# Optimization experiments

Hardware: AMD Instinct MI355X
Metric: run time of the kernel (lower is better)

Reference implementation:

```python
import jax, jax.numpy as jnp
import numpy as np

DIM = 256
N_STATE = 8
DT_RANK = 16  # ceil(dim/16)
D_CONV = 4
HIDDEN = 128  # dim * rank_ratio
EPS = 1e-6


def rmsnorm(x, w):
    # matches torch: x / (||x||_2 / sqrt(d) + eps) * w
    norm = jnp.sqrt(jnp.sum(x * x, axis=-1, keepdims=True))
    return x / (norm / np.sqrt(x.shape[-1]) + EPS) * w


def dwconv1d(x, w, b, pad_l, pad_r):
    # x: (b, l, c); w: (c, 1, k) depthwise
    out = jax.lax.conv_general_dilated(
        x.transpose(0, 2, 1), w, window_strides=(1,),
        padding=[(pad_l, pad_r)], dimension_numbers=('NCH', 'OIH', 'NCH'),
        feature_group_count=w.shape[0])
    return (out + b[None, :, None]).transpose(0, 2, 1)


def selective_scan(x, delta, A, Bm, Cm, D):
    # x, delta: (b,l,d); A: (d,n); Bm, Cm: (b,l,n); D: (d,)
    dA = jnp.exp(delta[..., None] * A)                     # (b,l,d,n)
    dBx = (delta * x)[..., None] * Bm[:, :, None, :]       # (b,l,d,n)

    def step(h, inp):
        dA_t, dBx_t, C_t = inp
        h = dA_t * h + dBx_t                               # (b,d,n)
        y = jnp.einsum('bdn,bn->bd', h, C_t)
        return h, y

    h0 = jnp.zeros((x.shape[0],) + A.shape, dtype=x.dtype)
    _, ys = jax.lax.scan(step, h0,
                         (dA.transpose(1, 0, 2, 3), dBx.transpose(1, 0, 2, 3),
                          Cm.transpose(1, 0, 2)))
    return ys.transpose(1, 0, 2) + x * D                   # (b,l,d)


def mamba_branch(x, ctx, conv_w, conv_b, xproj_w, dtproj_w, dtproj_b, A_log, D):
    xc = jax.nn.silu(dwconv1d(x, conv_w, conv_b, D_CONV - 1, 0))  # causal conv
    x_dbl = ctx @ xproj_w.T                                  # (b,l,r+2n)
    dt, Bm, Cm = jnp.split(x_dbl, [DT_RANK, DT_RANK + N_STATE], axis=-1)
    delta = jax.nn.softplus(dt @ dtproj_w.T + dtproj_b)
    A = -jnp.exp(A_log)
    return selective_scan(xc, delta, A, Bm, Cm, D)


def setup_inputs() -> dict:
    key = jax.random.key(0)
    ks = jax.random.split(key, 24)
    B, L, D = 4, 64 * 64, DIM
    s = 0.02
    A_log_init = jnp.log(jnp.broadcast_to(jnp.arange(1, N_STATE + 1, dtype=jnp.float32), (D, N_STATE)))
    dt_bias = jnp.full((D,), jnp.log(jnp.expm1(0.01)), dtype=jnp.float32)
    inp = {
        'x0': jax.random.normal(ks[0], (B, L, D), jnp.float32),
        'x1': jax.random.normal(ks[1], (B, L, D), jnp.float32),
        'w_norm0': jnp.ones((D,), jnp.float32),
        'w_norm1': jnp.ones((D,), jnp.float32),
        'in_proj_w': jax.random.normal(ks[2], (2 * D, D), jnp.float32) * s,
        'conv_w_f': jax.random.normal(ks[3], (D, 1, D_CONV), jnp.float32) * 0.3,
        'conv_b_f': jnp.zeros((D,), jnp.float32),
        'xproj_w_f': jax.random.normal(ks[4], (DT_RANK + 2 * N_STATE, D), jnp.float32) * s,
        'dtproj_w_f': jax.random.normal(ks[5], (D, DT_RANK), jnp.float32) * 0.1,
        'dtproj_b_f': dt_bias,
        'A_log_f': A_log_init,
        'D_f': jnp.ones((D,), jnp.float32),
        'conv_w_bw': jax.random.normal(ks[6], (D, 1, D_CONV), jnp.float32) * 0.3,
        'conv_b_bw': jnp.zeros((D,), jnp.float32),
        'xproj_w_bw': jax.random.normal(ks[7], (DT_RANK + 2 * N_STATE, D), jnp.float32) * s,
        'dtproj_w_bw': jax.random.normal(ks[8], (D, DT_RANK), jnp.float32) * 0.1,
        'dtproj_b_bw': dt_bias,
        'A_log_bw': A_log_init,
        'D_bw': jnp.ones((D,), jnp.float32),
        'norm_y_w': jnp.ones((D,), jnp.float32),
        'out_proj_w': jax.random.normal(ks[9], (D, D), jnp.float32) * s,
        'fc1_w': jax.random.normal(ks[10], (HIDDEN, D), jnp.float32) * s,
        'dw_w': jax.random.normal(ks[11], (HIDDEN, 1, 3), jnp.float32) * 0.3,
        'dw_b': jnp.zeros((HIDDEN,), jnp.float32),
        'fc2_w': jax.random.normal(ks[12], (D, HIDDEN), jnp.float32) * s,
    }
    return inp


def reference(x0, x1, w_norm0, w_norm1, in_proj_w, conv_w_f, conv_b_f, xproj_w_f,
              dtproj_w_f, dtproj_b_f, A_log_f, D_f, conv_w_bw, conv_b_bw,
              xproj_w_bw, dtproj_w_bw, dtproj_b_bw, A_log_bw, D_bw, norm_y_w,
              out_proj_w, fc1_w, dw_w, dw_b, fc2_w):
    residual = x0
    h0 = rmsnorm(x0, w_norm0)
    h1 = rmsnorm(x1, w_norm1)
    # cross-Mamba: main stream x0 -> x,z; extra_emb x1 -> dt/B/C
    xz = h0 @ in_proj_w.T
    xin, z = jnp.split(xz, 2, axis=-1)
    y_f = mamba_branch(xin, h1, conv_w_f, conv_b_f, xproj_w_f, dtproj_w_f,
                       dtproj_b_f, A_log_f, D_f)
    y_b = jnp.flip(mamba_branch(jnp.flip(xin, 1), jnp.flip(h1, 1), conv_w_bw,
                                conv_b_bw, xproj_w_bw, dtproj_w_bw, dtproj_b_bw,
                                A_log_bw, D_bw), 1)
    y = (y_f + y_b) * 0.5          # if_devide_out=True (bidirectional)
    y = rmsnorm(y, norm_y_w)       # use_norm=True
    y = y * jax.nn.silu(z)
    x = y @ out_proj_w.T + residual
    # LowRankFeedForward (dropout = identity at eval)
    m = x @ fc1_w.T
    m = jax.nn.silu(dwconv1d(m, dw_w, dw_b, 1, 1))
    m = m @ fc2_w.T
    return x + m
```

## Files before the change

kernel.cpp:

```cpp
#include <hip/hip_runtime.h>
#include <math.h>
#include <cstddef>

#define BB 4
#define LL 4096
#define DD 256
#define NST 8
#define RANK 16
#define HID 128
#define BL (BB*LL)
#define BLD ((size_t)BL*DD)
#define CH 256
#define CLEN 16
#define XZS 512

typedef __bf16 bf16x8 __attribute__((ext_vector_type(8)));
typedef float  f32x4  __attribute__((ext_vector_type(4)));

__device__ __forceinline__ float siluf(float x){ return x / (1.f + __expf(-x)); }
__device__ __forceinline__ float softplus_fast(float x){
  float r = __logf(1.f + __expf(x));
  return x > 15.f ? x : r;
}
__device__ __forceinline__ unsigned short f2bf(float x){
  union { float f; unsigned u; } v; v.f = x;
  unsigned r = v.u + 0x7fffu + ((v.u >> 16) & 1u);
  return (unsigned short)(r >> 16);
}
__device__ __forceinline__ float bf2f(unsigned short u){
  union { unsigned u32; float f; } c; c.u32 = ((unsigned)u) << 16;
  return c.f;
}

#define GLD16(gp, lp) __builtin_amdgcn_global_load_lds( \
    (const __attribute__((address_space(1))) unsigned int*)(gp), \
    (__attribute__((address_space(3))) unsigned int*)(lp), 16, 0, 0)

#define LDSG(base, row, gq) \
  (*(const bf16x8*)((base) + ((((row) << 3) + ((gq) ^ ((row) & 7))) << 3)))

__global__ __launch_bounds__(256) void pre_kernel(
    const float* __restrict__ x0, const float* __restrict__ w0, unsigned short* __restrict__ o0b,
    const float* __restrict__ x1, const float* __restrict__ w1, unsigned short* __restrict__ o1b,
    const float* __restrict__ sA,
    const float* __restrict__ s0, const float* __restrict__ s1,
    const float* __restrict__ s2, const float* __restrict__ s3,
    const float* __restrict__ s4,
    unsigned short* __restrict__ d1, unsigned short* __restrict__ d2)
{
  int blk = blockIdx.x;
  if (blk < 8192){
    const float* x; const float* w; unsigned short* o; size_t tok;
    int wv = threadIdx.x >> 6, lane = threadIdx.x & 63;
    if (blk < 4096){ x = x0; w = w0; o = o0b; tok = (size_t)blk*4 + wv; }
    else           { x = x1; w = w1; o = o1b; tok = (size_t)(blk-4096)*4 + wv; }
    float4 v = ((const float4*)(x + tok*DD))[lane];
    float s = v.x*v.x + v.y*v.y + v.z*v.z + v.w*v.w;
    #pragma unroll
    for (int m = 1; m < 64; m <<= 1) s += __shfl_xor(s, m, 64);
    float scale = 1.f / (sqrtf(s) * (1.f/16.f) + 1e-6f);
    float4 wvv = ((const float4*)w)[lane];
    ushort4 r;
    r.x = f2bf(v.x*scale*wvv.x); r.y = f2bf(v.y*scale*wvv.y);
    r.z = f2bf(v.z*scale*wvv.z); r.w = f2bf(v.w*scale*wvv.w);
    ((ushort4*)(o + tok*DD))[lane] = r;
    return;
  }
  int i = (blk - 8192)*256 + threadIdx.x;
  if (i >= 278528) return;
  if (i < 131072){ d1[i] = f2bf(sA[i]); return; }
  int j = i - 131072;
  float v;
  if (j < 8192)        v = s0[j];
  else if (j < 16384)  v = s1[j - 8192];
  else if (j < 81920)  v = s2[j - 16384];
  else if (j < 114688) v = s3[j - 81920];
  else                 v = s4[j - 114688];
  d2[j] = f2bf(v);
}

template<int EPI>
__global__ __launch_bounds__(256) void gemm_mfma(
    const unsigned short* __restrict__ A, const unsigned short* __restrict__ Bw,
    float* __restrict__ C, const float* __restrict__ Add,
    unsigned short* __restrict__ Cb, int M, int ldc, int K)
{
  constexpr int BK = 64;
  __shared__ __align__(16) unsigned short AsL[64*64];
  __shared__ __align__(16) unsigned short BsL[64*64];
  int tid  = threadIdx.x;
  int row0 = blockIdx.x * 64;
  int col0 = blockIdx.y * 64;
  int wave = tid >> 6, lane = tid & 63;
  int wm = (wave >> 1) * 32, wn = (wave & 1) * 32;
  int lm = lane & 15, kq = lane >> 4;

  int q0 = wave*128 + lane, q1 = q0 + 64;
  int ra = q0 >> 3, ga = (q0 & 7) ^ (ra & 7);
  int rb = q1 >> 3, gb = (q1 & 7) ^ (rb & 7);
  const unsigned short* A0 = A  + (size_t)(row0 + ra)*K + ga*8;
  const unsigned short* A1 = A  + (size_t)(row0 + rb)*K + gb*8;
  const unsigned short* B0 = Bw + (size_t)(col0 + ra)*K + ga*8;
  const unsigned short* B1 = Bw + (size_t)(col0 + rb)*K + gb*8;
  unsigned short* lA0 = AsL + wave*1024;
  unsigned short* lB0 = BsL + wave*1024;

  f32x4 acc[2][2];
  #pragma unroll
  for (int i = 0; i < 2; i++)
    #pragma unroll
    for (int j = 0; j < 2; j++) acc[i][j] = (f32x4){0.f,0.f,0.f,0.f};

  for (int k0 = 0; k0 < K; k0 += BK){
    GLD16(A0 + k0, lA0);       GLD16(A1 + k0, lA0 + 512);
    GLD16(B0 + k0, lB0);       GLD16(B1 + k0, lB0 + 512);
    __syncthreads();
    #pragma unroll
    for (int ks = 0; ks < 2; ks++){
      bf16x8 af[2], bfv[2];
      #pragma unroll
      for (int i = 0; i < 2; i++) af[i]  = LDSG(AsL, wm + i*16 + lm, ks*4 + kq);
      #pragma unroll
      for (int j = 0; j < 2; j++) bfv[j] = LDSG(BsL, wn + j*16 + lm, ks*4 + kq);
      #pragma unroll
      for (int i = 0; i < 2; i++)
        #pragma unroll
        for (int j = 0; j < 2; j++)
          acc[i][j] = __builtin_amdgcn_mfma_f32_16x16x32_bf16(af[i], bfv[j], acc[i][j], 0, 0, 0);
    }
    __syncthreads();
  }

  #pragma unroll
  for (int i = 0; i < 2; i++){
    int rbase = row0 + wm + i*16 + kq*4;
    #pragma unroll
    for (int j = 0; j < 2; j++){
      int col = col0 + wn + j*16 + lm;
      #pragma unroll
      for (int r = 0; r < 4; r++){
        size_t idx = (size_t)(rbase + r)*ldc + col;
        float v = acc[i][j][r];
        if constexpr (EPI == 2) v += Add[idx];
        if constexpr (EPI != 3) C[idx] = v;
        if constexpr (EPI == 3) Cb[idx] = f2bf(v);
      }
    }
  }
}

__global__ __launch_bounds__(256) void gemm_xzxp(
    const unsigned short* __restrict__ A0i, const unsigned short* __restrict__ A1i,
    const unsigned short* __restrict__ B0i, const unsigned short* __restrict__ B1i,
    unsigned short* __restrict__ Cxz, float* __restrict__ Cxd)
{
  constexpr int BK = 64, K = 256;
  __shared__ __align__(16) unsigned short AsL[64*64];
  __shared__ __align__(16) unsigned short BsL[64*64];
  int tid  = threadIdx.x;
  bool xp  = (blockIdx.y == 8);
  const unsigned short* A  = xp ? A1i : A0i;
  const unsigned short* Bw = xp ? B1i : B0i;
  int row0 = blockIdx.x * 64;
  int col0 = xp ? 0 : blockIdx.y * 64;
  int wave = tid >> 6, lane = tid & 63;
  int wm = (wave >> 1) * 32, wn = (wave & 1) * 32;
  int lm = lane & 15, kq = lane >> 4;

  int q0 = wave*128 + lane, q1 = q0 + 64;
  int ra = q0 >> 3, ga = (q0 & 7) ^ (ra & 7);
  int rb = q1 >> 3, gb = (q1 & 7) ^ (rb & 7);
  const unsigned short* A0 = A  + (size_t)(row0 + ra)*K + ga*8;
  const unsigned short* A1 = A  + (size_t)(row0 + rb)*K + gb*8;
  const unsigned short* B0 = Bw + (size_t)(col0 + ra)*K + ga*8;
  const unsigned short* B1 = Bw + (size_t)(col0 + rb)*K + gb*8;
  unsigned short* lA0 = AsL + wave*1024;
  unsigned short* lB0 = BsL + wave*1024;

  f32x4 acc[2][2];
  #pragma unroll
  for (int i = 0; i < 2; i++)
    #pragma unroll
    for (int j = 0; j < 2; j++) acc[i][j] = (f32x4){0.f,0.f,0.f,0.f};

  for (int k0 = 0; k0 < K; k0 += BK){
    GLD16(A0 + k0, lA0);       GLD16(A1 + k0, lA0 + 512);
    GLD16(B0 + k0, lB0);       GLD16(B1 + k0, lB0 + 512);
    __syncthreads();
    #pragma unroll
    for (int ks = 0; ks < 2; ks++){
      bf16x8 af[2], bfv[2];
      #pragma unroll
      for (int i = 0; i < 2; i++) af[i]  = LDSG(AsL, wm + i*16 + lm, ks*4 + kq);
      #pragma unroll
      for (int j = 0; j < 2; j++) bfv[j] = LDSG(BsL, wn + j*16 + lm, ks*4 + kq);
      #pragma unroll
      for (int i = 0; i < 2; i++)
        #pragma unroll
        for (int j = 0; j < 2; j++)
          acc[i][j] = __builtin_amdgcn_mfma_f32_16x16x32_bf16(af[i], bfv[j], acc[i][j], 0, 0, 0);
    }
    __syncthreads();
  }

  #pragma unroll
  for (int i = 0; i < 2; i++){
    int rbase = row0 + wm + i*16 + kq*4;
    #pragma unroll
    for (int j = 0; j < 2; j++){
      int col = col0 + wn + j*16 + lm;
      #pragma unroll
      for (int r = 0; r < 4; r++){
        float v = acc[i][j][r];
        if (xp) Cxd[(size_t)(rbase + r)*64  + col] = v;
        else    Cxz[(size_t)(rbase + r)*XZS + col] = f2bf(v);
      }
    }
  }
}

__global__ __launch_bounds__(256) void gemm_fc1(
    const float* __restrict__ A, const unsigned short* __restrict__ Bw,
    float* __restrict__ C)
{
  constexpr int BK = 64, PAD = 8, K = 256, LDC = 128;
  __shared__ __align__(16) unsigned short As[64][BK+PAD];
  __shared__ __align__(16) unsigned short BsL[64*64];
  int tid  = threadIdx.x;
  int row0 = blockIdx.x * 64;
  int col0 = blockIdx.y * 64;
  int wave = tid >> 6, lane = tid & 63;
  int wm = (wave >> 1) * 32, wn = (wave & 1) * 32;
  int lm = lane & 15, kq = lane >> 4;
  int sr = tid >> 2, sc16 = (tid & 3) * 16;

  int q0 = wave*128 + lane, q1 = q0 + 64;
  int ra = q0 >> 3, ga = (q0 & 7) ^ (ra & 7);
  int rb = q1 >> 3, gb = (q1 & 7) ^ (rb & 7);
  const unsigned short* B0 = Bw + (size_t)(col0 + ra)*K + ga*8;
  const unsigned short* B1 = Bw + (size_t)(col0 + rb)*K + gb*8;
  unsigned short* lB0 = BsL + wave*1024;

  f32x4 acc[2][2];
  #pragma unroll
  for (int i = 0; i < 2; i++)
    #pragma unroll
    for (int j = 0; j < 2; j++) acc[i][j] = (f32x4){0.f,0.f,0.f,0.f};

  for (int k0 = 0; k0 < K; k0 += BK){
    GLD16(B0 + k0, lB0);       GLD16(B1 + k0, lB0 + 512);
    const float* ap = &A[(size_t)(row0 + sr)*K + k0 + sc16];
    #pragma unroll
    for (int q = 0; q < 4; q++){
      float4 f = *(const float4*)(ap + q*4);
      ushort4 u; u.x = f2bf(f.x); u.y = f2bf(f.y); u.z = f2bf(f.z); u.w = f2bf(f.w);
      *(ushort4*)&As[sr][sc16 + q*4] = u;
    }
    __syncthreads();
    #pragma unroll
    for (int ks = 0; ks < 2; ks++){
      bf16x8 af[2], bfv[2];
      #pragma unroll
      for (int i = 0; i < 2; i++) af[i]  = *(const bf16x8*)&As[wm + i*16 + lm][ks*32 + kq*8];
      #pragma unroll
      for (int j = 0; j < 2; j++) bfv[j] = LDSG(BsL, wn + j*16 + lm, ks*4 + kq);
      #pragma unroll
      for (int i = 0; i < 2; i++)
        #pragma unroll
        for (int j = 0; j < 2; j++)
          acc[i][j] = __builtin_amdgcn_mfma_f32_16x16x32_bf16(af[i], bfv[j], acc[i][j], 0, 0, 0);
    }
    __syncthreads();
  }

  #pragma unroll
  for (int i = 0; i < 2; i++){
    int rbase = row0 + wm + i*16 + kq*4;
    #pragma unroll
    for (int j = 0; j < 2; j++){
      int col = col0 + wn + j*16 + lm;
      #pragma unroll
      for (int r = 0; r < 4; r++)
        C[(size_t)(rbase + r)*LDC + col] = acc[i][j][r];
    }
  }
}

__global__ __launch_bounds__(256) void gemm_fc2dw(
    const float* __restrict__ m1, const unsigned short* __restrict__ Bw,
    const float* __restrict__ dww, const float* __restrict__ dwb,
    float* __restrict__ C)
{
  constexpr int BK = 64, PAD = 8, K = 128, LDC = 256;
  __shared__ __align__(16) unsigned short As[64][BK+PAD];
  __shared__ __align__(16) unsigned short BsL[64*64];
  __shared__ float wS[HID*3];
  __shared__ float bS[HID];
  int tid  = threadIdx.x;
  if (tid < HID){
    bS[tid] = dwb[tid];
    wS[tid*3+0] = dww[tid*3+0];
    wS[tid*3+1] = dww[tid*3+1];
    wS[tid*3+2] = dww[tid*3+2];
  }
  __syncthreads();

  int row0 = blockIdx.x * 64;
  int col0 = blockIdx.y * 64;
  int wave = tid >> 6, lane = tid & 63;
  int wm = (wave >> 1) * 32, wn = (wave & 1) * 32;
  int lm = lane & 15, kq = lane >> 4;
  int r16 = tid >> 4, cc = (tid & 15) * 4;

  int q0 = wave*128 + lane, q1 = q0 + 64;
  int ra = q0 >> 3, ga = (q0 & 7) ^ (ra & 7);
  int rb = q1 >> 3, gb = (q1 & 7) ^ (rb & 7);
  const unsigned short* B0 = Bw + (size_t)(col0 + ra)*K + ga*8;
  const unsigned short* B1 = Bw + (size_t)(col0 + rb)*K + gb*8;
  unsigned short* lB0 = BsL + wave*1024;

  f32x4 acc[2][2];
  #pragma unroll
  for (int i = 0; i < 2; i++)
    #pragma unroll
    for (int j = 0; j < 2; j++) acc[i][j] = (f32x4){0.f,0.f,0.f,0.f};

  for (int k0 = 0; k0 < K; k0 += BK){
    GLD16(B0 + k0, lB0);       GLD16(B1 + k0, lB0 + 512);
    #pragma unroll
    for (int pp = 0; pp < 4; pp++){
      int r = pp*16 + r16;
      int t = row0 + r;
      int tl = t & (LL-1);
      int c = k0 + cc;
      const float* mrow = &m1[(size_t)t*HID + c];
      float4 vm = *(const float4*)mrow;
      float4 vp = (tl > 0)      ? *(const float4*)(mrow - HID) : (float4){0,0,0,0};
      float4 vn = (tl < LL-1)   ? *(const float4*)(mrow + HID) : (float4){0,0,0,0};
      float a0 = bS[c+0] + wS[(c+0)*3]*vp.x + wS[(c+0)*3+1]*vm.x + wS[(c+0)*3+2]*vn.x;
      float a1 = bS[c+1] + wS[(c+1)*3]*vp.y + wS[(c+1)*3+1]*vm.y + wS[(c+1)*3+2]*vn.y;
      float a2 = bS[c+2] + wS[(c+2)*3]*vp.z + wS[(c+2)*3+1]*vm.z + wS[(c+2)*3+2]*vn.z;
      float a3 = bS[c+3] + wS[(c+3)*3]*vp.w + wS[(c+3)*3+1]*vm.w + wS[(c+3)*3+2]*vn.w;
      ushort4 u;
      u.x = f2bf(siluf(a0)); u.y = f2bf(siluf(a1));
      u.z = f2bf(siluf(a2)); u.w = f2bf(siluf(a3));
      *(ushort4*)&As[r][cc] = u;
    }
    __syncthreads();
    #pragma unroll
    for (int ks = 0; ks < 2; ks++){
      bf16x8 af[2], bfv[2];
      #pragma unroll
      for (int i = 0; i < 2; i++) af[i]  = *(const bf16x8*)&As[wm + i*16 + lm][ks*32 + kq*8];
      #pragma unroll
      for (int j = 0; j < 2; j++) bfv[j] = LDSG(BsL, wn + j*16 + lm, ks*4 + kq);
      #pragma unroll
      for (int i = 0; i < 2; i++)
        #pragma unroll
        for (int j = 0; j < 2; j++)
          acc[i][j] = __builtin_amdgcn_mfma_f32_16x16x32_bf16(af[i], bfv[j], acc[i][j], 0, 0, 0);
    }
    __syncthreads();
  }

  #pragma unroll
  for (int i = 0; i < 2; i++){
    int rbase = row0 + wm + i*16 + kq*4;
    #pragma unroll
    for (int j = 0; j < 2; j++){
      int col = col0 + wn + j*16 + lm;
      #pragma unroll
      for (int r = 0; r < 4; r++){
        size_t idx = (size_t)(rbase + r)*LDC + col;
        C[idx] = C[idx] + acc[i][j][r];
      }
    }
  }
}

__global__ __launch_bounds__(256) void front_kernel(
    const unsigned short* __restrict__ xz,
    const float* __restrict__ xd,
    const float* __restrict__ cwf, const float* __restrict__ cbf,
    const float* __restrict__ cwb, const float* __restrict__ cbb,
    const float* __restrict__ dtwf, const float* __restrict__ dtbf,
    const float* __restrict__ dtwb, const float* __restrict__ dtbb,
    const float* __restrict__ Alogf, const float* __restrict__ Alogb,
    const float* __restrict__ Dfp, const float* __restrict__ Dbp,
    unsigned int* __restrict__ xde,
    float* __restrict__ Sp, float* __restrict__ Hout)
{
  int chunk = blockIdx.x, b = blockIdx.y, dir = blockIdx.z;
  int s0 = chunk*CLEN;
  int d  = threadIdx.x;

  __shared__ float sdt[CLEN][16];
  __shared__ float sB [CLEN][8];
  __shared__ float sC [CLEN][8];
  #pragma unroll
  for (int e = threadIdx.x; e < CLEN*32; e += 256){
    int lt = e >> 5, col = e & 31;
    int pos = s0 + lt;
    int row = dir ? (LL-1-pos) : pos;
    float v = xd[((size_t)b*LL + row)*64 + dir*32 + col];
    if (col < 16)      sdt[lt][col]    = v;
    else if (col < 24) sB [lt][col-16] = v;
    else               sC [lt][col-24] = v;
  }
  __syncthreads();

  float4 cw = ((const float4*)(dir ? cwb : cwf))[d];
  float cb  = (dir ? cbb : cbf)[d];
  const float* dtw = (dir ? dtwb : dtwf) + d*RANK;
  float4 w0 = ((const float4*)dtw)[0], w1 = ((const float4*)dtw)[1];
  float4 w2 = ((const float4*)dtw)[2], w3 = ((const float4*)dtw)[3];
  float dtb = (dir ? dtbb : dtbf)[d];
  float Dd  = (dir ? Dbp : Dfp)[d];

  const unsigned short* xp = xz + (size_t)b*LL*XZS + d;
  #define LDX(pos) ((pos) >= 0 ? bf2f(xp[(size_t)(dir ? (LL-1-(pos)) : (pos))*XZS]) : 0.f)

  float xv[CLEN+3];
  xv[0] = LDX(s0-3); xv[1] = LDX(s0-2); xv[2] = LDX(s0-1);
  #pragma unroll
  for (int i = 0; i < CLEN; i++) xv[3+i] = LDX(s0+i);
  #undef LDX

  unsigned packX[CLEN];
  #pragma unroll
  for (int i = 0; i < CLEN; i++){
    float xc = cb;
    xc = fmaf(cw.x, xv[i],   xc); xc = fmaf(cw.y, xv[i+1], xc);
    xc = fmaf(cw.z, xv[i+2], xc); xc = fmaf(cw.w, xv[i+3], xc);
    xc = siluf(xc);
    const float* dt = &sdt[i][0];
    float de = dtb;
    de = fmaf(dt[0],w0.x, fmaf(dt[1],w0.y, fmaf(dt[2],w0.z, fmaf(dt[3],w0.w, de))));
    de = fmaf(dt[4],w1.x, fmaf(dt[5],w1.y, fmaf(dt[6],w1.z, fmaf(dt[7],w1.w, de))));
    de = fmaf(dt[8],w2.x, fmaf(dt[9],w2.y, fmaf(dt[10],w2.z, fmaf(dt[11],w2.w, de))));
    de = fmaf(dt[12],w3.x, fmaf(dt[13],w3.y, fmaf(dt[14],w3.z, fmaf(dt[15],w3.w, de))));
    de = softplus_fast(de);
    packX[i] = (unsigned)f2bf(xc) | ((unsigned)f2bf(de) << 16);
  }

  const float* Alog = dir ? Alogb : Alogf;
  float A[NST];
  bool fast = true;
  #pragma unroll
  for (int n = 0; n < NST; n++){
    A[n] = -__expf(Alog[d*NST + n]);
    fast = fast && (fabsf(A[n] + (float)(n+1)) < 1e-3f);
  }
  float h[NST];
  #pragma unroll
  for (int n = 0; n < NST; n++) h[n] = 0.f;
  float S = 0.f;

  unsigned int* xout = xde + ((size_t)(dir*BB + b)*LL + s0)*DD + d;

  if (fast){
    #pragma unroll
    for (int t = 0; t < CLEN; t++){
      unsigned pk = packX[t];
      float xc = bf2f((unsigned short)(pk & 0xffffu));
      float de = bf2f((unsigned short)(pk >> 16));
      S += de;
      float dux = de * xc;
      const float* Bv = &sB[t][0];
      const float* Cv = &sC[t][0];
      float e1 = __expf(-de);
      float dA = e1;
      float acc = xc * Dd;
      h[0] = fmaf(dA, h[0], dux*Bv[0]); acc = fmaf(h[0], Cv[0], acc); dA *= e1;
      h[1] = fmaf(dA, h[1], dux*Bv[1]); acc = fmaf(h[1], Cv[1], acc); dA *= e1;
      h[2] = fmaf(dA, h[2], dux*Bv[2]); acc = fmaf(h[2], Cv[2], acc); dA *= e1;
      h[3] = fmaf(dA, h[3], dux*Bv[3]); acc = fmaf(h[3], Cv[3], acc); dA *= e1;
      h[4] = fmaf(dA, h[4], dux*Bv[4]); acc = fmaf(h[4], Cv[4], acc); dA *= e1;
      h[5] = fmaf(dA, h[5], dux*Bv[5]); acc = fmaf(h[5], Cv[5], acc); dA *= e1;
      h[6] = fmaf(dA, h[6], dux*Bv[6]); acc = fmaf(h[6], Cv[6], acc); dA *= e1;
      h[7] = fmaf(dA, h[7], dux*Bv[7]); acc = fmaf(h[7], Cv[7], acc);
      xout[(size_t)t*DD] = (pk & 0xffff0000u) | (unsigned)f2bf(acc);
    }
  } else {
    #pragma unroll
    for (int t = 0; t < CLEN; t++){
      unsigned pk = packX[t];
      float xc = bf2f((unsigned short)(pk & 0xffffu));
      float de = bf2f((unsigned short)(pk >> 16));
      S += de;
      float dux = de * xc;
      const float* Bv = &sB[t][0];
      const float* Cv = &sC[t][0];
      float acc = xc * Dd;
      #pragma unroll
      for (int n = 0; n < NST; n++){
        h[n] = fmaf(__expf(de*A[n]), h[n], dux*Bv[n]);
        acc = fmaf(h[n], Cv[n], acc);
      }
      xout[(size_t)t*DD] = (pk & 0xffff0000u) | (unsigned)f2bf(acc);
    }
  }

  size_t ob = ((((size_t)dir*CH + chunk)*BB + b)*DD + d)*NST;
  float4 h0v, h1v;
  h0v.x=h[0]; h0v.y=h[1]; h0v.z=h[2]; h0v.w=h[3];
  h1v.x=h[4]; h1v.y=h[5]; h1v.z=h[6]; h1v.w=h[7];
  *(float4*)&Hout[ob]   = h0v; *(float4*)&Hout[ob+4] = h1v;
  Sp[((size_t)(dir*CH + chunk)*BB + b)*DD + d] = S;
}

__global__ __launch_bounds__(64) void scan_p2(
    const float* __restrict__ Sp, float* H,
    const float* __restrict__ Alogf, const float* __restrict__ Alogb)
{
  const int SEGC = CH/8;
  int blk = blockIdx.x;
  int d   = blk & (DD-1);
  int b   = (blk >> 8) & (BB-1);
  int dir = blk >> 10;
  int t   = threadIdx.x;
  int seg = t >> 3, n = t & 7;
  float A = -__expf((dir ? Alogb : Alogf)[d*NST + n]);

  const size_t sstr = (size_t)BB*DD;
  const size_t hstr = (size_t)BB*DD*NST;
  size_t sb = (size_t)dir*CH*sstr + (size_t)b*DD + d;
  size_t hb = (size_t)dir*CH*hstr + ((size_t)b*DD + d)*NST + n;
  int c0 = seg*SEGC;

  float pv[SEGC], hv[SEGC];
  #pragma unroll
  for (int k = 0; k < SEGC; k++){
    pv[k] = Sp[sb + (size_t)(c0+k)*sstr];
    hv[k] = H [hb + (size_t)(c0+k)*hstr];
  }
  float h = 0.f, Ss = 0.f;
  #pragma unroll
  for (int k = 0; k < SEGC; k++){
    Ss += pv[k];
    pv[k] = __expf(pv[k]*A);
    h = fmaf(pv[k], h, hv[k]);
  }
  float pi = __expf(Ss*A), hi = h;
  #pragma unroll
  for (int off = 8; off < 64; off <<= 1){
    float hprev = __shfl_up(hi, off, 64);
    float pprev = __shfl_up(pi, off, 64);
    if (t >= off){ hi = fmaf(pi, hprev, hi); pi *= pprev; }
  }
  float hin = __shfl_up(hi, 8, 64);
  h = (seg == 0) ? 0.f : hin;
  #pragma unroll
  for (int k = 0; k < SEGC; k++){
    size_t idx = hb + (size_t)(c0+k)*hstr;
    H[idx] = h;
    h = fmaf(pv[k], h, hv[k]);
  }
}

__global__ __launch_bounds__(256) void back_kernel(
    const unsigned int* __restrict__ xde,
    const float* __restrict__ xd,
    const float* __restrict__ Alogf, const float* __restrict__ Alogb,
    const float* __restrict__ Hin,
    const unsigned short* __restrict__ xz,
    const float* __restrict__ wn,
    unsigned short* __restrict__ outb)
{
  int c  = blockIdx.x, b = blockIdx.y;
  int cbk = CH-1-c;
  int d  = threadIdx.x;
  int T0 = c*CLEN;
  int Pb = cbk*CLEN;

  __shared__ float sCf[CLEN][8], sCb[CLEN][8];
  __shared__ float red[CLEN][4];
  __shared__ float sscale[CLEN];
  {
    int k  = threadIdx.x & 7;
    int lt = (threadIdx.x >> 3) & 15;
    if (threadIdx.x < 128)
      sCf[lt][k] = xd[((size_t)b*LL + T0 + lt)*64 + 24 + k];
    else
      sCb[lt][k] = xd[((size_t)b*LL + (T0 + 15 - lt))*64 + 56 + k];
  }
  __syncthreads();

  float Af[NST], Ab[NST];
  bool fast = true;
  #pragma unroll
  for (int n = 0; n < NST; n++){
    Af[n] = -__expf(Alogf[d*NST + n]);
    Ab[n] = -__expf(Alogb[d*NST + n]);
    fast = fast && (fabsf(Af[n] + (float)(n+1)) < 1e-3f)
                && (fabsf(Ab[n] + (float)(n+1)) < 1e-3f);
  }

  float vf[CLEN];

  {
    float hn[NST];
    size_t ib = (((size_t)c*BB + b)*DD + d)*NST;
    float4 a0 = *(const float4*)&Hin[ib];
    float4 a1 = *(const float4*)&Hin[ib+4];
    hn[0]=a0.x; hn[1]=a0.y; hn[2]=a0.z; hn[3]=a0.w;
    hn[4]=a1.x; hn[5]=a1.y; hn[6]=a1.z; hn[7]=a1.w;
    const unsigned int* p = xde + ((size_t)b*LL + T0)*DD + d;
    unsigned int pk[CLEN];
    #pragma unroll
    for (int t = 0; t < CLEN; t++) pk[t] = p[(size_t)t*DD];
    float S = 0.f;
    if (fast){
      #pragma unroll
      for (int t = 0; t < CLEN; t++){
        float y0 = bf2f((unsigned short)(pk[t] & 0xffffu));
        float de = bf2f((unsigned short)(pk[t] >> 16));
        S += de;
        float E = __expf(-S);
        float q = E;
        float corr = q * (hn[0]*sCf[t][0]);
        q *= E; corr = fmaf(q, hn[1]*sCf[t][1], corr);
        q *= E; corr = fmaf(q, hn[2]*sCf[t][2], corr);
        q *= E; corr = fmaf(q, hn[3]*sCf[t][3], corr);
        q *= E; corr = fmaf(q, hn[4]*sCf[t][4], corr);
        q *= E; corr = fmaf(q, hn[5]*sCf[t][5], corr);
        q *= E; corr = fmaf(q, hn[6]*sCf[t][6], corr);
        q *= E; corr = fmaf(q, hn[7]*sCf[t][7], corr);
        vf[t] = y0 + corr;
      }
    } else {
      #pragma unroll
      for (int t = 0; t < CLEN; t++){
        float y0 = bf2f((unsigned short)(pk[t] & 0xffffu));
        float de = bf2f((unsigned short)(pk[t] >> 16));
        S += de;
        float corr = 0.f;
        #pragma unroll
        for (int n = 0; n < NST; n++)
          corr = fmaf(__expf(S*Af[n]), hn[n]*sCf[t][n], corr);
        vf[t] = y0 + corr;
      }
    }
  }

  {
    float hn[NST];
    size_t ib = ((((size_t)CH + cbk)*BB + b)*DD + d)*NST;
    float4 a0 = *(const float4*)&Hin[ib];
    float4 a1 = *(const float4*)&Hin[ib+4];
    hn[0]=a0.x; hn[1]=a0.y; hn[2]=a0.z; hn[3]=a0.w;
    hn[4]=a1.x; hn[5]=a1.y; hn[6]=a1.z; hn[7]=a1.w;
    const unsigned int* p = xde + ((size_t)(BB + b)*LL + Pb)*DD + d;
    unsigned int pk[CLEN];
    #pragma unroll
    for (int t = 0; t < CLEN; t++) pk[t] = p[(size_t)t*DD];
    float S = 0.f;
    if (fast){
      #pragma unroll
      for (int t = 0; t < CLEN; t++){
        float y0 = bf2f((unsigned short)(pk[t] & 0xffffu));
        float de = bf2f((unsigned short)(pk[t] >> 16));
        S += de;
        float E = __expf(-S);
        float q = E;
        float corr = q * (hn[0]*sCb[t][0]);
        q *= E; corr = fmaf(q, hn[1]*sCb[t][1], corr);
        q *= E; corr = fmaf(q, hn[2]*sCb[t][2], corr);
        q *= E; corr = fmaf(q, hn[3]*sCb[t][3], corr);
        q *= E; corr = fmaf(q, hn[4]*sCb[t][4], corr);
        q *= E; corr = fmaf(q, hn[5]*sCb[t][5], corr);
        q *= E; corr = fmaf(q, hn[6]*sCb[t][6], corr);
        q *= E; corr = fmaf(q, hn[7]*sCb[t][7], corr);
        int j = 15 - t;
        vf[j] = 0.5f*(vf[j] + y0 + corr);
      }
    } else {
      #pragma unroll
      for (int t = 0; t < CLEN; t++){
        float y0 = bf2f((unsigned short)(pk[t] & 0xffffu));
        float de = bf2f((unsigned short)(pk[t] >> 16));
        S += de;
        float corr = 0.f;
        #pragma unroll
        for (int n = 0; n < NST; n++)
          corr = fmaf(__expf(S*Ab[n]), hn[n]*sCb[t][n], corr);
        int j = 15 - t;
        vf[j] = 0.5f*(vf[j] + y0 + corr);
      }
    }
  }

  int wave = d >> 6, lane = d & 63;
  #pragma unroll
  for (int j = 0; j < CLEN; j++){
    float s = vf[j]*vf[j];
    #pragma unroll
    for (int m = 1; m < 64; m <<= 1) s += __shfl_xor(s, m, 64);
    if (lane == 0) red[j][wave] = s;
  }
  __syncthreads();
  if (d < CLEN){
    float s = red[d][0] + red[d][1] + red[d][2] + red[d][3];
    sscale[d] = 1.f / (sqrtf(s)*(1.f/16.f) + 1e-6f);
  }
  __syncthreads();

  float wd = wn[d];
  #pragma unroll
  for (int j = 0; j < CLEN; j++){
    size_t tok = (size_t)b*LL + T0 + j;
    float z = bf2f(xz[tok*XZS + 256 + d]);
    outb[tok*DD + d] = f2bf(vf[j]*sscale[j]*wd*siluf(z));
  }
}

extern "C" void kernel_launch(void* const* d_in, const int* in_sizes, int n_in,
                              void* d_out, int out_size, void* d_ws, size_t ws_size,
                              hipStream_t stream)
{
  const float* x0        = (const float*)d_in[0];
  const float* x1        = (const float*)d_in[1];
  const float* w_norm0   = (const float*)d_in[2];
  const float* w_norm1   = (const float*)d_in[3];
  const float* in_proj_w = (const float*)d_in[4];
  const float* conv_w_f  = (const float*)d_in[5];
  const float* conv_b_f  = (const float*)d_in[6];
  const float* xproj_w_f = (const float*)d_in[7];
  const float* dtproj_w_f= (const float*)d_in[8];
  const float* dtproj_b_f= (const float*)d_in[9];
  const float* A_log_f   = (const float*)d_in[10];
  const float* D_f       = (const float*)d_in[11];
  const float* conv_w_bw = (const float*)d_in[12];
  const float* conv_b_bw = (const float*)d_in[13];
  const float* xproj_w_bw= (const float*)d_in[14];
  const float* dtproj_w_bw=(const float*)d_in[15];
  const float* dtproj_b_bw=(const float*)d_in[16];
  const float* A_log_bw  = (const float*)d_in[17];
  const float* D_bw      = (const float*)d_in[18];
  const float* norm_y_w  = (const float*)d_in[19];
  const float* out_proj_w= (const float*)d_in[20];
  const float* fc1_w     = (const float*)d_in[21];
  const float* dw_w      = (const float*)d_in[22];
  const float* dw_b      = (const float*)d_in[23];
  const float* fc2_w     = (const float*)d_in[24];
  float* out = (float*)d_out;
  float* ws  = (float*)d_ws;

  float* r0 = ws + 0*BLD;
  float* r1 = ws + 1*BLD;
  float* r2 = ws + 2*BLD;
  float* r3 = ws + 3*BLD;
  float* r4 = ws + 4*BLD;
  float* r5 = ws + 5*BLD;
  float* r6 = ws + 6*BLD;
  float* r7 = ws + 7*BLD;

  unsigned short* h0b   = (unsigned short*)r0;
  unsigned short* h1b   = (unsigned short*)r1;
  unsigned short* xz_b  = (unsigned short*)r2;
  float*          xd    = r3;
  unsigned int*   xde   = (unsigned int*)r4;
  unsigned short* wbuf1 = (unsigned short*)r6;
  float* Hout = r6;
  float* Hin  = Hout;
  const size_t SPLANE = (size_t)2*CH*BB*DD;
  float* Sp   = r7 + (BLD - SPLANE);
  unsigned short* ycomb_b = (unsigned short*)r0;
  unsigned short* wbuf2   = (unsigned short*)r7;
  unsigned short* wb_xp   = wbuf2;
  unsigned short* wb_out  = wbuf2 + 16384;
  unsigned short* wb_fc1  = wbuf2 + 81920;
  unsigned short* wb_fc2  = wbuf2 + 114688;
  float*          m1      = r4;

  pre_kernel<<<dim3(9280), 256, 0, stream>>>(
      x0, w_norm0, h0b, x1, w_norm1, h1b,
      in_proj_w, xproj_w_f, xproj_w_bw, out_proj_w, fc1_w, fc2_w, wbuf1, wbuf2);

  gemm_xzxp<<<dim3(BL/64, 9), 256, 0, stream>>>(
      h0b, h1b, wbuf1, wb_xp, xz_b, xd);

  front_kernel<<<dim3(CH, BB, 2), 256, 0, stream>>>(
      xz_b, xd, conv_w_f, conv_b_f, conv_w_bw, conv_b_bw,
      dtproj_w_f, dtproj_b_f, dtproj_w_bw, dtproj_b_bw,
      A_log_f, A_log_bw, D_f, D_bw, xde, Sp, Hout);

  scan_p2<<<dim3(2*BB*DD), 64, 0, stream>>>(Sp, Hout, A_log_f, A_log_bw);

  back_kernel<<<dim3(CH, BB), 256, 0, stream>>>(
      xde, xd, A_log_f, A_log_bw, Hin, xz_b, norm_y_w, ycomb_b);

  gemm_mfma<2><<<dim3(BL/64, 4), 256, 0, stream>>>(
      ycomb_b, wb_out, out, x0, nullptr, BL, 256, 256);

  gemm_fc1<<<dim3(BL/64, 2), 256, 0, stream>>>(out, wb_fc1, m1);

  gemm_fc2dw<<<dim3(BL/64, 4), 256, 0, stream>>>(m1, wb_fc2, dw_w, dw_b, out);
}
```

Baseline: 248.6 us.

## Fuse chunked scan phases into one persistent kernel with grid barriers

Merges the front (per-chunk local scan), the inter-chunk prefix pass and the back (correction + norm) kernels into a single 1024-block kernel that synchronises with software grid barriers. Per-chunk packed y/delta values stay in registers across the barriers instead of round-tripping through a global xde buffer, and two kernel launches are removed. It relies on all 1024 blocks being co-resident (launch_bounds 256,4), which risks deadlock if occupancy is lower, and it leaves most blocks idle during the middle phase and adds register pressure.

Result: slower. 670.1 us (+169.5%).

```diff
diff --git a/kernel.cpp b/kernel.cpp
--- a/kernel.cpp
+++ b/kernel.cpp
@@ -39,6 +39,24 @@
 #define LDSG(base, row, gq) \
   (*(const bf16x8*)((base) + ((((row) << 3) + ((gq) ^ ((row) & 7))) << 3)))
 
+__device__ __forceinline__ void grid_barrier(unsigned* cnt, unsigned* gen, unsigned nb){
+  __syncthreads();
+  if (threadIdx.x == 0){
+    __threadfence();
+    unsigned g = __hip_atomic_load(gen, __ATOMIC_RELAXED, __HIP_MEMORY_SCOPE_AGENT);
+    unsigned a = __hip_atomic_fetch_add(cnt, 1u, __ATOMIC_ACQ_REL, __HIP_MEMORY_SCOPE_AGENT);
+    if (a == nb - 1u){
+      __hip_atomic_store(cnt, 0u, __ATOMIC_RELAXED, __HIP_MEMORY_SCOPE_AGENT);
+      __hip_atomic_fetch_add(gen, 1u, __ATOMIC_RELEASE, __HIP_MEMORY_SCOPE_AGENT);
+    } else {
+      while (__hip_atomic_load(gen, __ATOMIC_ACQUIRE, __HIP_MEMORY_SCOPE_AGENT) == g)
+        __builtin_amdgcn_s_sleep(8);
+    }
+    __threadfence();
+  }
+  __syncthreads();
+}
+
 __global__ __launch_bounds__(256) void pre_kernel(
     const float* __restrict__ x0, const float* __restrict__ w0, unsigned short* __restrict__ o0b,
     const float* __restrict__ x1, const float* __restrict__ w1, unsigned short* __restrict__ o1b,
@@ -46,9 +64,11 @@
     const float* __restrict__ s0, const float* __restrict__ s1,
     const float* __restrict__ s2, const float* __restrict__ s3,
     const float* __restrict__ s4,
-    unsigned short* __restrict__ d1, unsigned short* __restrict__ d2)
+    unsigned short* __restrict__ d1, unsigned short* __restrict__ d2,
+    unsigned* __restrict__ bar)
 {
   int blk = blockIdx.x;
+  if (blk == 8192 && threadIdx.x < 2) bar[threadIdx.x] = 0;
   if (blk < 8192){
     const float* x; const float* w; unsigned short* o; size_t tok;
     int wv = threadIdx.x >> 6, lane = threadIdx.x & 63;
@@ -378,7 +398,7 @@
   }
 }
 
-__global__ __launch_bounds__(256) void front_kernel(
+__global__ __launch_bounds__(256, 4) void fused_scan(
     const unsigned short* __restrict__ xz,
     const float* __restrict__ xd,
     const float* __restrict__ cwf, const float* __restrict__ cbf,
@@ -387,205 +407,188 @@
     const float* __restrict__ dtwb, const float* __restrict__ dtbb,
     const float* __restrict__ Alogf, const float* __restrict__ Alogb,
     const float* __restrict__ Dfp, const float* __restrict__ Dbp,
-    unsigned int* __restrict__ xde,
-    float* __restrict__ Sp, float* __restrict__ Hout)
+    const float* __restrict__ wn,
+    unsigned short* __restrict__ outb,
+    float* __restrict__ Sp, float* H, unsigned* bar)
 {
-  int chunk = blockIdx.x, b = blockIdx.y, dir = blockIdx.z;
-  int s0 = chunk*CLEN;
-  int d  = threadIdx.x;
+  int blk = blockIdx.x;
+  int c   = blk >> 2;
+  int b   = blk & 3;
+  int d   = threadIdx.x;
+  int cbk = CH-1-c;
 
   __shared__ float sdt[CLEN][16];
   __shared__ float sB [CLEN][8];
-  __shared__ float sC [CLEN][8];
-  #pragma unroll
-  for (int e = threadIdx.x; e < CLEN*32; e += 256){
-    int lt = e >> 5, col = e & 31;
-    int pos = s0 + lt;
-    int row = dir ? (LL-1-pos) : pos;
-    float v = xd[((size_t)b*LL + row)*64 + dir*32 + col];
-    if (col < 16)      sdt[lt][col]    = v;
-    else if (col < 24) sB [lt][col-16] = v;
-    else               sC [lt][col-24] = v;
-  }
-  __syncthreads();
-
-  float4 cw = ((const float4*)(dir ? cwb : cwf))[d];
-  float cb  = (dir ? cbb : cbf)[d];
-  const float* dtw = (dir ? dtwb : dtwf) + d*RANK;
-  float4 w0 = ((const float4*)dtw)[0], w1 = ((const float4*)dtw)[1];
-  float4 w2 = ((const float4*)dtw)[2], w3 = ((const float4*)dtw)[3];
-  float dtb = (dir ? dtbb : dtbf)[d];
-  float Dd  = (dir ? Dbp : Dfp)[d];
-
-  const unsigned short* xp = xz + (size_t)b*LL*XZS + d;
-  #define LDX(pos) ((pos) >= 0 ? bf2f(xp[(size_t)(dir ? (LL-1-(pos)) : (pos))*XZS]) : 0.f)
-
-  float xv[CLEN+3];
-  xv[0] = LDX(s0-3); xv[1] = LDX(s0-2); xv[2] = LDX(s0-1);
-  #pragma unroll
-  for (int i = 0; i < CLEN; i++) xv[3+i] = LDX(s0+i);
-  #undef LDX
-
-  unsigned packX[CLEN];
-  #pragma unroll
-  for (int i = 0; i < CLEN; i++){
-    float xc = cb;
-    xc = fmaf(cw.x, xv[i],   xc); xc = fmaf(cw.y, xv[i+1], xc);
-    xc = fmaf(cw.z, xv[i+2], xc); xc = fmaf(cw.w, xv[i+3], xc);
-    xc = siluf(xc);
-    const float* dt = &sdt[i][0];
-    float de = dtb;
-    de = fmaf(dt[0],w0.x, fmaf(dt[1],w0.y, fmaf(dt[2],w0.z, fmaf(dt[3],w0.w, de))));
-    de = fmaf(dt[4],w1.x, fmaf(dt[5],w1.y, fmaf(dt[6],w1.z, fmaf(dt[7],w1.w, de))));
-    de = fmaf(dt[8],w2.x, fmaf(dt[9],w2.y, fmaf(dt[10],w2.z, fmaf(dt[11],w2.w, de))));
-    de = fmaf(dt[12],w3.x, fmaf(dt[13],w3.y, fmaf(dt[14],w3.z, fmaf(dt[15],w3.w, de))));
-    de = softplus_fast(de);
-    packX[i] = (unsigned)f2bf(xc) | ((unsigned)f2bf(de) << 16);
-  }
-
-  const float* Alog = dir ? Alogb : Alogf;
-  float A[NST];
-  bool fast = true;
-  #pragma unroll
-  for (int n = 0; n < NST; n++){
-    A[n] = -__expf(Alog[d*NST + n]);
-    fast = fast && (fabsf(A[n] + (float)(n+1)) < 1e-3f);
-  }
-  float h[NST];
-  #pragma unroll
-  for (int n = 0; n < NST; n++) h[n] = 0.f;
-  float S = 0.f;
-
-  unsigned int* xout = xde + ((size_t)(dir*BB + b)*LL + s0)*DD + d;
-
-  if (fast){
-    #pragma unroll
-    for (int t = 0; t < CLEN; t++){
-      unsigned pk = packX[t];
-      float xc = bf2f((unsigned short)(pk & 0xffffu));
-      float de = bf2f((unsigned short)(pk >> 16));
-      S += de;
-      float dux = de * xc;
-      const float* Bv = &sB[t][0];
-      const float* Cv = &sC[t][0];
-      float e1 = __expf(-de);
-      float dA = e1;
-      float acc = xc * Dd;
-      h[0] = fmaf(dA, h[0], dux*Bv[0]); acc = fmaf(h[0], Cv[0], acc); dA *= e1;
-      h[1] = fmaf(dA, h[1], dux*Bv[1]); acc = fmaf(h[1], Cv[1], acc); dA *= e1;
-      h[2] = fmaf(dA, h[2], dux*Bv[2]); acc = fmaf(h[2], Cv[2], acc); dA *= e1;
-      h[3] = fmaf(dA, h[3], dux*Bv[3]); acc = fmaf(h[3], Cv[3], acc); dA *= e1;
-      h[4] = fmaf(dA, h[4], dux*Bv[4]); acc = fmaf(h[4], Cv[4], acc); dA *= e1;
-      h[5] = fmaf(dA, h[5], dux*Bv[5]); acc = fmaf(h[5], Cv[5], acc); dA *= e1;
-      h[6] = fmaf(dA, h[6], dux*Bv[6]); acc = fmaf(h[6], Cv[6], acc); dA *= e1;
-      h[7] = fmaf(dA, h[7], dux*Bv[7]); acc = fmaf(h[7], Cv[7], acc);
-      xout[(size_t)t*DD] = (pk & 0xffff0000u) | (unsigned)f2bf(acc);
-    }
-  } else {
-    #pragma unroll
-    for (int t = 0; t < CLEN; t++){
-      unsigned pk = packX[t];
-      float xc = bf2f((unsigned short)(pk & 0xffffu));
-      float de = bf2f((unsigned short)(pk >> 16));
-      S += de;
-      float dux = de * xc;
-      const float* Bv = &sB[t][0];
-      const float* Cv = &sC[t][0];
-      float acc = xc * Dd;
-      #pragma unroll
-      for (int n = 0; n < NST; n++){
-        h[n] = fmaf(__expf(de*A[n]), h[n], dux*Bv[n]);
-        acc = fmaf(h[n], Cv[n], acc);
-      }
-      xout[(size_t)t*DD] = (pk & 0xffff0000u) | (unsigned)f2bf(acc);
-    }
-  }
-
-  size_t ob = ((((size_t)dir*CH + chunk)*BB + b)*DD + d)*NST;
-  float4 h0v, h1v;
-  h0v.x=h[0]; h0v.y=h[1]; h0v.z=h[2]; h0v.w=h[3];
-  h1v.x=h[4]; h1v.y=h[5]; h1v.z=h[6]; h1v.w=h[7];
-  *(float4*)&Hout[ob]   = h0v; *(float4*)&Hout[ob+4] = h1v;
-  Sp[((size_t)(dir*CH + chunk)*BB + b)*DD + d] = S;
-}
-
-__global__ __launch_bounds__(64) void scan_p2(
-    const float* __restrict__ Sp, float* H,
-    const float* __restrict__ Alogf, const float* __restrict__ Alogb)
-{
-  const int SEGC = CH/8;
-  int blk = blockIdx.x;
-  int d   = blk & (DD-1);
-  int b   = (blk >> 8) & (BB-1);
-  int dir = blk >> 10;
-  int t   = threadIdx.x;
-  int seg = t >> 3, n = t & 7;
-  float A = -__expf((dir ? Alogb : Alogf)[d*NST + n]);
-
-  const size_t sstr = (size_t)BB*DD;
-  const size_t hstr = (size_t)BB*DD*NST;
-  size_t sb = (size_t)dir*CH*sstr + (size_t)b*DD + d;
-  size_t hb = (size_t)dir*CH*hstr + ((size_t)b*DD + d)*NST + n;
-  int c0 = seg*SEGC;
-
-  float pv[SEGC], hv[SEGC];
-  #pragma unroll
-  for (int k = 0; k < SEGC; k++){
-    pv[k] = Sp[sb + (size_t)(c0+k)*sstr];
-    hv[k] = H [hb + (size_t)(c0+k)*hstr];
-  }
-  float h = 0.f, Ss = 0.f;
-  #pragma unroll
-  for (int k = 0; k < SEGC; k++){
-    Ss += pv[k];
-    pv[k] = __expf(pv[k]*A);
-    h = fmaf(pv[k], h, hv[k]);
-  }
-  float pi = __expf(Ss*A), hi = h;
-  #pragma unroll
-  for (int off = 8; off < 64; off <<= 1){
-    float hprev = __shfl_up(hi, off, 64);
-    float pprev = __shfl_up(pi, off, 64);
-    if (t >= off){ hi = fmaf(pi, hprev, hi); pi *= pprev; }
-  }
-  float hin = __shfl_up(hi, 8, 64);
-  h = (seg == 0) ? 0.f : hin;
-  #pragma unroll
-  for (int k = 0; k < SEGC; k++){
-    size_t idx = hb + (size_t)(c0+k)*hstr;
-    H[idx] = h;
-    h = fmaf(pv[k], h, hv[k]);
-  }
-}
-
-__global__ __launch_bounds__(256) void back_kernel(
-    const unsigned int* __restrict__ xde,
-    const float* __restrict__ xd,
-    const float* __restrict__ Alogf, const float* __restrict__ Alogb,
-    const float* __restrict__ Hin,
-    const unsigned short* __restrict__ xz,
-    const float* __restrict__ wn,
-    unsigned short* __restrict__ outb)
-{
-  int c  = blockIdx.x, b = blockIdx.y;
-  int cbk = CH-1-c;
-  int d  = threadIdx.x;
-  int T0 = c*CLEN;
-  int Pb = cbk*CLEN;
-
-  __shared__ float sCf[CLEN][8], sCb[CLEN][8];
+  __shared__ float sCf[CLEN][8];
+  __shared__ float sCb[CLEN][8];
   __shared__ float red[CLEN][4];
   __shared__ float sscale[CLEN];
+
+  unsigned pkF[CLEN], pkB[CLEN];
+
+  auto run_front = [&](int chunk, int dirv, float (&sCx)[CLEN][8], unsigned* pk){
+    int s0 = chunk*CLEN;
+    __syncthreads();
+    #pragma unroll
+    for (int e = d; e < CLEN*32; e += 256){
+      int lt = e >> 5, col = e & 31;
+      int pos = s0 + lt;
+      int row = dirv ? (LL-1-pos) : pos;
+      float v = xd[((size_t)b*LL + row)*64 + dirv*32 + col];
+      if (col < 16)      sdt[lt][col]    = v;
+      else if (col < 24) sB [lt][col-16] = v;
+      else               sCx[lt][col-24] = v;
+    }
+    __syncthreads();
+
+    float4 cw = ((const float4*)(dirv ? cwb : cwf))[d];
+    float cb  = (dirv ? cbb : cbf)[d];
+    const float* dtw = (dirv ? dtwb : dtwf) + d*RANK;
+    float4 w0 = ((const float4*)dtw)[0], w1 = ((const float4*)dtw)[1];
+    float4 w2 = ((const float4*)dtw)[2], w3 = ((const float4*)dtw)[3];
+    float dtb = (dirv ? dtbb : dtbf)[d];
+    float Dd  = (dirv ? Dbp : Dfp)[d];
+
+    const unsigned short* xp = xz + (size_t)b*LL*XZS + d;
+    #define LDX(pos) ((pos) >= 0 ? bf2f(xp[(size_t)(dirv ? (LL-1-(pos)) : (pos))*XZS]) : 0.f)
+    float xv[CLEN+3];
+    xv[0] = LDX(s0-3); xv[1] = LDX(s0-2); xv[2] = LDX(s0-1);
+    #pragma unroll
+    for (int i = 0; i < CLEN; i++) xv[3+i] = LDX(s0+i);
+    #undef LDX
+
+    #pragma unroll
+    for (int i = 0; i < CLEN; i++){
+      float xc = cb;
+      xc = fmaf(cw.x, xv[i],   xc); xc = fmaf(cw.y, xv[i+1], xc);
+      xc = fmaf(cw.z, xv[i+2], xc); xc = fmaf(cw.w, xv[i+3], xc);
+      xc = siluf(xc);
+      const float* dt = &sdt[i][0];
+      float de = dtb;
+      de = fmaf(dt[0],w0.x, fmaf(dt[1],w0.y, fmaf(dt[2],w0.z, fmaf(dt[3],w0.w, de))));
+      de = fmaf(dt[4],w1.x, fmaf(dt[5],w1.y, fmaf(dt[6],w1.z, fmaf(dt[7],w1.w, de))));
+      de = fmaf(dt[8],w2.x, fmaf(dt[9],w2.y, fmaf(dt[10],w2.z, fmaf(dt[11],w2.w, de))));
+      de = fmaf(dt[12],w3.x, fmaf(dt[13],w3.y, fmaf(dt[14],w3.z, fmaf(dt[15],w3.w, de))));
+      de = softplus_fast(de);
+      pk[i] = (unsigned)f2bf(xc) | ((unsigned)f2bf(de) << 16);
+    }
+
+    const float* Alog = dirv ? Alogb : Alogf;
+    float A[NST];
+    bool fast = true;
+    #pragma unroll
+    for (int n = 0; n < NST; n++){
+      A[n] = -__expf(Alog[d*NST + n]);
+      fast = fast && (fabsf(A[n] + (float)(n+1)) < 1e-3f);
+    }
+    float h[NST];
+    #pragma unroll
+    for (int n = 0; n < NST; n++) h[n] = 0.f;
+    float S = 0.f;
+
+    if (fast){
+      #pragma unroll
+      for (int t = 0; t < CLEN; t++){
+        unsigned pkv = pk[t];
+        float xc = bf2f((unsigned short)(pkv & 0xffffu));
+        float de = bf2f((unsigned short)(pkv >> 16));
+        S += de;
+        float dux = de * xc;
+        const float* Bv = &sB[t][0];
+        const float* Cv = &sCx[t][0];
+        float e1 = __expf(-de);
+        float dA = e1;
+        float acc = xc * Dd;
+        h[0] = fmaf(dA, h[0], dux*Bv[0]); acc = fmaf(h[0], Cv[0], acc); dA *= e1;
+        h[1] = fmaf(dA, h[1], dux*Bv[1]); acc = fmaf(h[1], Cv[1], acc); dA *= e1;
+        h[2] = fmaf(dA, h[2], dux*Bv[2]); acc = fmaf(h[2], Cv[2], acc); dA *= e1;
+        h[3] = fmaf(dA, h[3], dux*Bv[3]); acc = fmaf(h[3], Cv[3], acc); dA *= e1;
+        h[4] = fmaf(dA, h[4], dux*Bv[4]); acc = fmaf(h[4], Cv[4], acc); dA *= e1;
+        h[5] = fmaf(dA, h[5], dux*Bv[5]); acc = fmaf(h[5], Cv[5], acc); dA *= e1;
+        h[6] = fmaf(dA, h[6], dux*Bv[6]); acc = fmaf(h[6], Cv[6], acc); dA *= e1;
+        h[7] = fmaf(dA, h[7], dux*Bv[7]); acc = fmaf(h[7], Cv[7], acc);
+        pk[t] = (pkv & 0xffff0000u) | (unsigned)f2bf(acc);
+      }
+    } else {
+      #pragma unroll
+      for (int t = 0; t < CLEN; t++){
+        unsigned pkv = pk[t];
+        float xc = bf2f((unsigned short)(pkv & 0xffffu));
+        float de = bf2f((unsigned short)(pkv >> 16));
+        S += de;
+        float dux = de * xc;
+        const float* Bv = &sB[t][0];
+        const float* Cv = &sCx[t][0];
+        float acc = xc * Dd;
+        #pragma unroll
+        for (int n = 0; n < NST; n++){
+          h[n] = fmaf(__expf(de*A[n]), h[n], dux*Bv[n]);
+          acc = fmaf(h[n], Cv[n], acc);
+        }
+        pk[t] = (pkv & 0xffff0000u) | (unsigned)f2bf(acc);
+      }
+    }
+
+    size_t ob = ((((size_t)dirv*CH + chunk)*BB + b)*DD + d)*NST;
+    float4 h0v, h1v;
+    h0v.x=h[0]; h0v.y=h[1]; h0v.z=h[2]; h0v.w=h[3];
+    h1v.x=h[4]; h1v.y=h[5]; h1v.z=h[6]; h1v.w=h[7];
+    *(float4*)&H[ob]   = h0v; *(float4*)&H[ob+4] = h1v;
+    Sp[((size_t)(dirv*CH + chunk)*BB + b)*DD + d] = S;
+  };
+
+  run_front(c,   0, sCf, pkF);
+  run_front(cbk, 1, sCb, pkB);
+
+  grid_barrier(bar, bar+1, CH*BB);
+
   {
-    int k  = threadIdx.x & 7;
-    int lt = (threadIdx.x >> 3) & 15;
-    if (threadIdx.x < 128)
-      sCf[lt][k] = xd[((size_t)b*LL + T0 + lt)*64 + 24 + k];
-    else
-      sCb[lt][k] = xd[((size_t)b*LL + (T0 + 15 - lt))*64 + 56 + k];
-  }
-  __syncthreads();
-
+    int wave = d >> 6, lane = d & 63;
+    if (wave < 2){
+      const int SEGC = CH/8;
+      int u   = blk*2 + wave;
+      int d2  = u & (DD-1);
+      int b2  = (u >> 8) & (BB-1);
+      int dir2= u >> 10;
+      int seg = lane >> 3, n = lane & 7;
+      float A = -__expf((dir2 ? Alogb : Alogf)[d2*NST + n]);
+      const size_t sstr = (size_t)BB*DD;
+      const size_t hstr = (size_t)BB*DD*NST;
+      size_t sb = (size_t)dir2*CH*sstr + (size_t)b2*DD + d2;
+      size_t hb = (size_t)dir2*CH*hstr + ((size_t)b2*DD + d2)*NST + n;
+      int c0 = seg*SEGC;
+
+      float hv[SEGC];
+      float h = 0.f, Ss = 0.f;
+      #pragma unroll
+      for (int k = 0; k < SEGC; k++){
+        float s = Sp[sb + (size_t)(c0+k)*sstr];
+        hv[k]  = H [hb + (size_t)(c0+k)*hstr];
+        Ss += s;
+        h = fmaf(__expf(s*A), h, hv[k]);
+      }
+      float pi = __expf(Ss*A), hi = h;
+      #pragma unroll
+      for (int off = 8; off < 64; off <<= 1){
+        float hprev = __shfl_up(hi, off, 64);
+        float pprev = __shfl_up(pi, off, 64);
+        if (lane >= off){ hi = fmaf(pi, hprev, hi); pi *= pprev; }
+      }
+      float hin = __shfl_up(hi, 8, 64);
+      h = (seg == 0) ? 0.f : hin;
+      #pragma unroll
+      for (int k = 0; k < SEGC; k++){
+        float s = Sp[sb + (size_t)(c0+k)*sstr];
+        size_t hix = hb + (size_t)(c0+k)*hstr;
+        H[hix] = h;
+        h = fmaf(__expf(s*A), h, hv[k]);
+      }
+    }
+  }
+
+  grid_barrier(bar, bar+1, CH*BB);
+
+  int T0 = c*CLEN;
   float Af[NST], Ab[NST];
   bool fast = true;
   #pragma unroll
@@ -601,20 +604,16 @@
   {
     float hn[NST];
     size_t ib = (((size_t)c*BB + b)*DD + d)*NST;
-    float4 a0 = *(const float4*)&Hin[ib];
-    float4 a1 = *(const float4*)&Hin[ib+4];
+    float4 a0 = *(const float4*)&H[ib];
+    float4 a1 = *(const float4*)&H[ib+4];
     hn[0]=a0.x; hn[1]=a0.y; hn[2]=a0.z; hn[3]=a0.w;
     hn[4]=a1.x; hn[5]=a1.y; hn[6]=a1.z; hn[7]=a1.w;
-    const unsigned int* p = xde + ((size_t)b*LL + T0)*DD + d;
-    unsigned int pk[CLEN];
-    #pragma unroll
-    for (int t = 0; t < CLEN; t++) pk[t] = p[(size_t)t*DD];
     float S = 0.f;
     if (fast){
       #pragma unroll
       for (int t = 0; t < CLEN; t++){
-        float y0 = bf2f((unsigned short)(pk[t] & 0xffffu));
-        float de = bf2f((unsigned short)(pk[t] >> 16));
+        float y0 = bf2f((unsigned short)(pkF[t] & 0xffffu));
+        float de = bf2f((unsigned short)(pkF[t] >> 16));
         S += de;
         float E = __expf(-S);
         float q = E;
@@ -631,8 +630,8 @@
     } else {
       #pragma unroll
       for (int t = 0; t < CLEN; t++){
-        float y0 = bf2f((unsigned short)(pk[t] & 0xffffu));
-        float de = bf2f((unsigned short)(pk[t] >> 16));
+        float y0 = bf2f((unsigned short)(pkF[t] & 0xffffu));
+        float de = bf2f((unsigned short)(pkF[t] >> 16));
         S += de;
         float corr = 0.f;
         #pragma unroll
@@ -646,20 +645,16 @@
   {
     float hn[NST];
     size_t ib = ((((size_t)CH + cbk)*BB + b)*DD + d)*NST;
-    float4 a0 = *(const float4*)&Hin[ib];
-    float4 a1 = *(const float4*)&Hin[ib+4];
+    float4 a0 = *(const float4*)&H[ib];
+    float4 a1 = *(const float4*)&H[ib+4];
     hn[0]=a0.x; hn[1]=a0.y; hn[2]=a0.z; hn[3]=a0.w;
     hn[4]=a1.x; hn[5]=a1.y; hn[6]=a1.z; hn[7]=a1.w;
-    const unsigned int* p = xde + ((size_t)(BB + b)*LL + Pb)*DD + d;
-    unsigned int pk[CLEN];
-    #pragma unroll
-    for (int t = 0; t < CLEN; t++) pk[t] = p[(size_t)t*DD];
     float S = 0.f;
     if (fast){
       #pragma unroll
       for (int t = 0; t < CLEN; t++){
-        float y0 = bf2f((unsigned short)(pk[t] & 0xffffu));
-        float de = bf2f((unsigned short)(pk[t] >> 16));
+        float y0 = bf2f((unsigned short)(pkB[t] & 0xffffu));
+        float de = bf2f((unsigned short)(pkB[t] >> 16));
         S += de;
         float E = __expf(-S);
         float q = E;
@@ -677,8 +672,8 @@
     } else {
       #pragma unroll
       for (int t = 0; t < CLEN; t++){
-        float y0 = bf2f((unsigned short)(pk[t] & 0xffffu));
-        float de = bf2f((unsigned short)(pk[t] >> 16));
+        float y0 = bf2f((unsigned short)(pkB[t] & 0xffffu));
+        float de = bf2f((unsigned short)(pkB[t] >> 16));
         S += de;
         float corr = 0.f;
         #pragma unroll
@@ -751,7 +746,6 @@
   float* r2 = ws + 2*BLD;
   float* r3 = ws + 3*BLD;
   float* r4 = ws + 4*BLD;
-  float* r5 = ws + 5*BLD;
   float* r6 = ws + 6*BLD;
   float* r7 = ws + 7*BLD;
 
@@ -759,12 +753,11 @@
   unsigned short* h1b   = (unsigned short*)r1;
   unsigned short* xz_b  = (unsigned short*)r2;
   float*          xd    = r3;
-  unsigned int*   xde   = (unsigned int*)r4;
   unsigned short* wbuf1 = (unsigned short*)r6;
-  float* Hout = r6;
-  float* Hin  = Hout;
+  float* H = r6;
   const size_t SPLANE = (size_t)2*CH*BB*DD;
   float* Sp   = r7 + (BLD - SPLANE);
+  unsigned* bar = (unsigned*)(Sp - 4);
   unsigned short* ycomb_b = (unsigned short*)r0;
   unsigned short* wbuf2   = (unsigned short*)r7;
   unsigned short* wb_xp   = wbuf2;
@@ -775,20 +768,16 @@
 
   pre_kernel<<<dim3(9280), 256, 0, stream>>>(
       x0, w_norm0, h0b, x1, w_norm1, h1b,
-      in_proj_w, xproj_w_f, xproj_w_bw, out_proj_w, fc1_w, fc2_w, wbuf1, wbuf2);
+      in_proj_w, xproj_w_f, xproj_w_bw, out_proj_w, fc1_w, fc2_w, wbuf1, wbuf2,
+      bar);
 
   gemm_xzxp<<<dim3(BL/64, 9), 256, 0, stream>>>(
       h0b, h1b, wbuf1, wb_xp, xz_b, xd);
 
-  front_kernel<<<dim3(CH, BB, 2), 256, 0, stream>>>(
+  fused_scan<<<dim3(CH*BB), 256, 0, stream>>>(
       xz_b, xd, conv_w_f, conv_b_f, conv_w_bw, conv_b_bw,
       dtproj_w_f, dtproj_b_f, dtproj_w_bw, dtproj_b_bw,
-      A_log_f, A_log_bw, D_f, D_bw, xde, Sp, Hout);
-
-  scan_p2<<<dim3(2*BB*DD), 64, 0, stream>>>(Sp, Hout, A_log_f, A_log_bw);
-
-  back_kernel<<<dim3(CH, BB), 256, 0, stream>>>(
-      xde, xd, A_log_f, A_log_bw, Hin, xz_b, norm_y_w, ycomb_b);
+      A_log_f, A_log_bw, D_f, D_bw, norm_y_w, ycomb_b, Sp, H, bar);
 
   gemm_mfma<2><<<dim3(BL/64, 4), 256, 0, stream>>>(
       ycomb_b, wb_out, out, x0, nullptr, BL, 256, 256);
```
